# Performance work log

Hardware: AMD Instinct MI355X
Metric: run time of the kernel (lower is better)

## Reference

```python
import jax, jax.numpy as jnp
import numpy as np

TEMPERATURE = 0.07
EPS = 1e-8  # torch CosineSimilarity eps
N, D = 8192, 128

def setup_inputs() -> dict:
    key = jax.random.key(0)
    k1, k2, k3 = jax.random.split(key, 3)
    features = jax.random.normal(k1, (N, D), dtype=jnp.float32)
    positive_mask = jax.random.randint(k2, (N, N), 0, 2, dtype=jnp.int32)
    negative_mask = jax.random.randint(k3, (N, N), 0, 2, dtype=jnp.int32)
    return {"features": features, "positive_mask": positive_mask, "negative_mask": negative_mask}

def reference(features, positive_mask, negative_mask):
    n = positive_mask.shape[0]
    # remove self-contrast (zero the diagonal)
    not_self = 1.0 - jnp.eye(n, dtype=features.dtype)
    pos_m = positive_mask.astype(features.dtype) * not_self
    neg_m = negative_mask.astype(features.dtype) * not_self
    # cosine similarity: normalize once, then Gram matrix [N, N]
    norms = jnp.maximum(jnp.linalg.norm(features, axis=-1, keepdims=True), EPS)
    fn = features / norms
    sim = jnp.exp(jnp.einsum('id,jd->ij', fn, fn) / TEMPERATURE)  # [N, N]
    pos = jnp.sum(sim * pos_m, axis=1)
    neg = jnp.sum(sim * neg_m, axis=1)
    loss = -jnp.mean(jnp.log(pos / (pos + neg)))
    return loss
```

## Files before the change

kernel.cpp:

```cpp
#include <hip/hip_runtime.h>
#include <hip/hip_bf16.h>

#define N 8192
#define D 128
#define INV_T 14.285714285714286f

typedef __bf16 v8bf __attribute__((ext_vector_type(8)));
typedef float  v4f  __attribute__((ext_vector_type(4)));

__global__ __launch_bounds__(256) void normalize_kernel(
    const float* __restrict__ f, __bf16* __restrict__ out)
{
    int gwave = (blockIdx.x * blockDim.x + threadIdx.x) >> 6;
    int lane  = threadIdx.x & 63;
    const float2 v = *reinterpret_cast<const float2*>(f + (size_t)gwave * D + lane * 2);
    float ss = v.x * v.x + v.y * v.y;
    #pragma unroll
    for (int m = 32; m; m >>= 1) ss += __shfl_xor(ss, m);
    float norm = fmaxf(sqrtf(ss), 1e-8f);
    float inv  = 1.0f / norm;
    __bf16* o = out + (size_t)gwave * D + lane * 2;
    o[0] = (__bf16)(v.x * inv);
    o[1] = (__bf16)(v.y * inv);
}

__global__ __launch_bounds__(256) void supcon_main(
    const __bf16* __restrict__ F,
    const int* __restrict__ pmask, const int* __restrict__ nmask,
    float* __restrict__ pos, float* __restrict__ neg)
{
    const int tid  = threadIdx.x;
    const int lane = tid & 63;
    const int wid  = tid >> 6;
    const int wr   = wid >> 1, wc = wid & 1;
    const int i0   = blockIdx.y * 128 + wr * 64;
    const int j0   = blockIdx.x * 128 + wc * 64;
    const int r    = lane & 15;
    const int q    = lane >> 4;

    v4f acc[4][4];
    #pragma unroll
    for (int m = 0; m < 4; ++m)
        #pragma unroll
        for (int n = 0; n < 4; ++n) acc[m][n] = (v4f)0.0f;

    #pragma unroll
    for (int ks = 0; ks < 4; ++ks) {
        v8bf a[4], b[4];
        #pragma unroll
        for (int m = 0; m < 4; ++m)
            a[m] = *reinterpret_cast<const v8bf*>(F + (size_t)(i0 + m * 16 + r) * D + ks * 32 + q * 8);
        #pragma unroll
        for (int n = 0; n < 4; ++n)
            b[n] = *reinterpret_cast<const v8bf*>(F + (size_t)(j0 + n * 16 + r) * D + ks * 32 + q * 8);
        #pragma unroll
        for (int m = 0; m < 4; ++m)
            #pragma unroll
            for (int n = 0; n < 4; ++n)
                acc[m][n] = __builtin_amdgcn_mfma_f32_16x16x32_bf16(a[m], b[n], acc[m][n], 0, 0, 0);
    }

    #pragma unroll
    for (int m = 0; m < 4; ++m) {
        #pragma unroll
        for (int v = 0; v < 4; ++v) {
            const int gi = i0 + m * 16 + q * 4 + v;
            const int* __restrict__ prow = pmask + (size_t)gi * N + j0 + r;
            const int* __restrict__ nrow = nmask + (size_t)gi * N + j0 + r;
            float p = 0.0f, g = 0.0f;
            #pragma unroll
            for (int n = 0; n < 4; ++n) {
                const int gj = j0 + n * 16 + r;
                int pm = prow[n * 16];
                int nm = nrow[n * 16];
                float s = acc[m][n][v];
                float e = __expf(s * INV_T);
                e = (gi != gj) ? e : 0.0f;
                p = fmaf((float)pm, e, p);
                g = fmaf((float)nm, e, g);
            }
            #pragma unroll
            for (int msk = 1; msk < 16; msk <<= 1) {
                p += __shfl_xor(p, msk);
                g += __shfl_xor(g, msk);
            }
            if (r == 0) {
                atomicAdd(&pos[gi], p);
                atomicAdd(&neg[gi], g);
            }
        }
    }
}

__global__ __launch_bounds__(1024) void finalize_kernel(
    const float* __restrict__ pos, const float* __restrict__ neg, float* __restrict__ out)
{
    __shared__ float sm[16];
    int tid = threadIdx.x;
    float acc = 0.0f;
    for (int i = tid; i < N; i += 1024) {
        float p = pos[i], g = neg[i];
        acc += logf(p / (p + g));
    }
    #pragma unroll
    for (int m = 32; m; m >>= 1) acc += __shfl_xor(acc, m);
    if ((tid & 63) == 0) sm[tid >> 6] = acc;
    __syncthreads();
    if (tid == 0) {
        float t = 0.0f;
        #pragma unroll
        for (int w = 0; w < 16; ++w) t += sm[w];
        out[0] = -t * (1.0f / (float)N);
    }
}

extern "C" void kernel_launch(void* const* d_in, const int* in_sizes, int n_in,
                              void* d_out, int out_size, void* d_ws, size_t ws_size,
                              hipStream_t stream) {
    const float* feat  = (const float*)d_in[0];
    const int*   pmask = (const int*)d_in[1];
    const int*   nmask = (const int*)d_in[2];
    float* out = (float*)d_out;

    char* ws = (char*)d_ws;
    __bf16* fnb = (__bf16*)ws;
    float*  pos = (float*)(ws + (size_t)2 * 1024 * 1024);
    float*  neg = pos + N;

    hipMemsetAsync(pos, 0, 2 * N * sizeof(float), stream);

    normalize_kernel<<<dim3(N / 4), 256, 0, stream>>>(feat, fnb);

    dim3 grid(N / 128, N / 128);
    supcon_main<<<grid, 256, 0, stream>>>(fnb, pmask, nmask, pos, neg);

    finalize_kernel<<<1, 1024, 0, stream>>>(pos, neg, out);
}
```

Before: 582.4 us.

## Stage exp tile in LDS to read masks with coalesced int4 loads

The exponentiated similarity tile is written to shared memory as bf16, and the tile is then re-read row-wise so each lane loads contiguous int4 chunks of the positive and negative masks. Before this, the mask reads followed the MFMA output layout, which gave 16-lane scattered scalar loads. The kernel is bound by reading two 256MB int masks, so coalesced vector loads should raise achieved bandwidth. The cost is extra LDS traffic, a block barrier, 32-wide shuffle reductions, and rounding the exp values to bf16 before the masked sums.

```diff
diff --git a/kernel.cpp b/kernel.cpp
--- a/kernel.cpp
+++ b/kernel.cpp
@@ -4,8 +4,10 @@
 #define N 8192
 #define D 128
 #define INV_T 14.285714285714286f
+#define LDS_PITCH 136
 
 typedef __bf16 v8bf __attribute__((ext_vector_type(8)));
+typedef __bf16 v4bf __attribute__((ext_vector_type(4)));
 typedef float  v4f  __attribute__((ext_vector_type(4)));
 
 __global__ __launch_bounds__(256) void normalize_kernel(
@@ -17,8 +19,7 @@
     float ss = v.x * v.x + v.y * v.y;
     #pragma unroll
     for (int m = 32; m; m >>= 1) ss += __shfl_xor(ss, m);
-    float norm = fmaxf(sqrtf(ss), 1e-8f);
-    float inv  = 1.0f / norm;
+    float inv = 1.0f / fmaxf(sqrtf(ss), 1e-8f);
     __bf16* o = out + (size_t)gwave * D + lane * 2;
     o[0] = (__bf16)(v.x * inv);
     o[1] = (__bf16)(v.y * inv);
@@ -29,12 +30,16 @@
     const int* __restrict__ pmask, const int* __restrict__ nmask,
     float* __restrict__ pos, float* __restrict__ neg)
 {
+    __shared__ __bf16 E[128 * LDS_PITCH];
+
     const int tid  = threadIdx.x;
     const int lane = tid & 63;
     const int wid  = tid >> 6;
     const int wr   = wid >> 1, wc = wid & 1;
-    const int i0   = blockIdx.y * 128 + wr * 64;
-    const int j0   = blockIdx.x * 128 + wc * 64;
+    const int i0   = blockIdx.y * 128;
+    const int j0   = blockIdx.x * 128;
+    const int iw   = i0 + wr * 64;
+    const int jw   = j0 + wc * 64;
     const int r    = lane & 15;
     const int q    = lane >> 4;
 
@@ -49,10 +54,10 @@
         v8bf a[4], b[4];
         #pragma unroll
         for (int m = 0; m < 4; ++m)
-            a[m] = *reinterpret_cast<const v8bf*>(F + (size_t)(i0 + m * 16 + r) * D + ks * 32 + q * 8);
+            a[m] = *reinterpret_cast<const v8bf*>(F + (size_t)(iw + m * 16 + r) * D + ks * 32 + q * 8);
         #pragma unroll
         for (int n = 0; n < 4; ++n)
-            b[n] = *reinterpret_cast<const v8bf*>(F + (size_t)(j0 + n * 16 + r) * D + ks * 32 + q * 8);
+            b[n] = *reinterpret_cast<const v8bf*>(F + (size_t)(jw + n * 16 + r) * D + ks * 32 + q * 8);
         #pragma unroll
         for (int m = 0; m < 4; ++m)
             #pragma unroll
@@ -60,34 +65,47 @@
                 acc[m][n] = __builtin_amdgcn_mfma_f32_16x16x32_bf16(a[m], b[n], acc[m][n], 0, 0, 0);
     }
 
+    const bool diag = (blockIdx.x == blockIdx.y);
     #pragma unroll
     for (int m = 0; m < 4; ++m) {
         #pragma unroll
-        for (int v = 0; v < 4; ++v) {
-            const int gi = i0 + m * 16 + q * 4 + v;
-            const int* __restrict__ prow = pmask + (size_t)gi * N + j0 + r;
-            const int* __restrict__ nrow = nmask + (size_t)gi * N + j0 + r;
-            float p = 0.0f, g = 0.0f;
+        for (int n = 0; n < 4; ++n) {
+            const int colL = wc * 64 + n * 16 + r;
             #pragma unroll
-            for (int n = 0; n < 4; ++n) {
-                const int gj = j0 + n * 16 + r;
-                int pm = prow[n * 16];
-                int nm = nrow[n * 16];
-                float s = acc[m][n][v];
-                float e = __expf(s * INV_T);
-                e = (gi != gj) ? e : 0.0f;
-                p = fmaf((float)pm, e, p);
-                g = fmaf((float)nm, e, g);
+            for (int v = 0; v < 4; ++v) {
+                const int rowL = wr * 64 + m * 16 + q * 4 + v;
+                float e = __expf(acc[m][n][v] * INV_T);
+                if (diag && rowL == colL) e = 0.0f;
+                E[rowL * LDS_PITCH + colL] = (__bf16)e;
             }
-            #pragma unroll
-            for (int msk = 1; msk < 16; msk <<= 1) {
-                p += __shfl_xor(p, msk);
-                g += __shfl_xor(g, msk);
-            }
-            if (r == 0) {
-                atomicAdd(&pos[gi], p);
-                atomicAdd(&neg[gi], g);
-            }
+        }
+    }
+    __syncthreads();
+
+    const int half = lane >> 5;
+    const int c    = lane & 31;
+    #pragma unroll
+    for (int it = 0; it < 16; ++it) {
+        const int row = wid * 32 + it * 2 + half;
+        const int gi  = i0 + row;
+        const size_t base = (size_t)gi * N + j0 + c * 4;
+        const int4 pm = *reinterpret_cast<const int4*>(pmask + base);
+        const int4 nm = *reinterpret_cast<const int4*>(nmask + base);
+        const v4bf ev = *reinterpret_cast<const v4bf*>(&E[row * LDS_PITCH + c * 4]);
+        const float e0 = (float)ev[0], e1 = (float)ev[1];
+        const float e2 = (float)ev[2], e3 = (float)ev[3];
+        float p = fmaf((float)pm.x, e0, fmaf((float)pm.y, e1,
+                  fmaf((float)pm.z, e2, (float)pm.w * e3)));
+        float g = fmaf((float)nm.x, e0, fmaf((float)nm.y, e1,
+                  fmaf((float)nm.z, e2, (float)nm.w * e3)));
+        #pragma unroll
+        for (int msk = 1; msk < 32; msk <<= 1) {
+            p += __shfl_xor(p, msk);
+            g += __shfl_xor(g, msk);
+        }
+        if (c == 0) {
+            atomicAdd(&pos[gi], p);
+            atomicAdd(&neg[gi], g);
         }
     }
 }
```

New measurement: 582.9 us. No clear change (+0.1%).
